# Kernel optimization log

Hardware: AMD Instinct MI355X
Metric: run time of the kernel (lower is better)

Reference implementation:

```python
import jax, jax.numpy as jnp
import numpy as np

VOCAB = 1_000_000   # vocabulary_size (num_classes)
EMB = 128           # embedding_size
NEG = 512           # number_of_negative_samples (num_sampled)
NTRUE = 1           # positive_samples (num_true)
BATCH = 16384


def _log_uniform_prob(ids, vocab):
    # TF LogUniformCandidateSampler: P(c) = (log(c+2) - log(c+1)) / log(vocab+1)
    c = ids.astype(jnp.float32)
    return (jnp.log(c + 2.0) - jnp.log(c + 1.0)) / jnp.log(float(vocab) + 1.0)


def _expected_count(ids, vocab, num_sampled):
    # unique sampling with num_sampled tries: E[count] = 1 - (1-p)^num_sampled
    p = _log_uniform_prob(ids, vocab)
    return -jnp.expm1(num_sampled * jnp.log1p(-p))


def _sigmoid_ce(logits, z):
    # stable sigmoid cross-entropy with label value z
    return jnp.maximum(logits, 0.0) - logits * z + jnp.log1p(jnp.exp(-jnp.abs(logits)))


def setup_inputs() -> dict:
    key = jax.random.key(0)
    k1, k2, k3, k4 = jax.random.split(key, 4)
    return {
        "predictions": jax.random.normal(k1, (BATCH, EMB), jnp.float32),
        "weights": jax.random.normal(k2, (VOCAB, EMB), jnp.float32) * 0.02,
        "biases": jnp.zeros((VOCAB,), jnp.float32),
        "labels": jax.random.randint(k3, (BATCH, NTRUE), 0, VOCAB, dtype=jnp.int64),
        "sampled": jax.random.randint(k4, (NEG,), 0, VOCAB, dtype=jnp.int64),
    }


def reference(predictions, weights, biases, labels, sampled):
    # --- true class logits: gather rows then batched dot ---
    true_w = weights[labels]                         # [B, T, E]
    true_b = biases[labels]                          # [B, T]
    true_logits = jnp.einsum('be,bte->bt', predictions, true_w) + true_b
    true_logits = true_logits - jnp.log(_expected_count(labels, VOCAB, NEG))

    # --- sampled (negative) class logits: shared across batch ---
    samp_logits = predictions @ weights[sampled].T + biases[sampled]  # [B, S]
    samp_logits = samp_logits - jnp.log(_expected_count(sampled, VOCAB, NEG))

    # --- sigmoid cross-entropy; true label value is 1/num_true ---
    loss_true = _sigmoid_ce(true_logits, jnp.float32(1.0 / NTRUE)).sum(axis=-1)
    loss_samp = _sigmoid_ce(samp_logits, jnp.float32(0.0)).sum(axis=-1)
    return jnp.mean(loss_true + loss_samp)
```

## Files before the change

kernel.cpp:

```cpp
#include <hip/hip_runtime.h>
#include <hip/hip_bf16.h>

#define VOCAB 1000000
#define EMB 128
#define NEG 512
#define BATCH 16384

#define BM 64
#define BN 64
#define KE 160
#define LDSTR 168

#define NMAIN ((BATCH / BM) * (NEG / BN))
#define NTRUE_BLK (BATCH / 4)
#define NPART (NMAIN + NTRUE_BLK)

typedef __attribute__((ext_vector_type(8))) short bf16x8;
typedef __attribute__((ext_vector_type(4))) float f32x4;

static __device__ __forceinline__ unsigned short f2bf(float f) {
    union { __hip_bfloat16 b; unsigned short u; } cv;
    cv.b = __float2bfloat16(f);
    return cv.u;
}
static __device__ __forceinline__ float bf2f(unsigned short u) {
    union { unsigned short u; __hip_bfloat16 b; } cv;
    cv.u = u;
    return __bfloat162float(cv.b);
}

static __device__ __forceinline__ float neg_log_expected(int c) {
    float cf = (float)c;
    float p = log1pf(1.0f / (cf + 1.0f)) / logf((float)VOCAB + 1.0f);
    float E = -expm1f((float)NEG * log1pf(-p));
    return -logf(E);
}

__global__ __launch_bounds__(64) void prep_k(const float* __restrict__ weights,
                                             const float* __restrict__ biases,
                                             const int* __restrict__ sampled,
                                             unsigned short* __restrict__ swe) {
    int s = blockIdx.x;
    int t = threadIdx.x;
    int sid = sampled[s];
    unsigned short* row = swe + (size_t)s * KE;
    if (t < 32) {
        const float4* src = (const float4*)(weights + (size_t)sid * EMB);
        float4 v = src[t];
        uint2 p;
        p.x = (unsigned)f2bf(v.x) | ((unsigned)f2bf(v.y) << 16);
        p.y = (unsigned)f2bf(v.z) | ((unsigned)f2bf(v.w) << 16);
        *(uint2*)(row + t * 4) = p;
    } else {
        int slot = 128 + (t - 32);
        unsigned short v = 0;
        if (slot <= 129) {
            float c = biases[sid] + neg_log_expected(sid);
            unsigned short hi = f2bf(c);
            v = (slot == 128) ? hi : f2bf(c - bf2f(hi));
        }
        row[slot] = v;
    }
}

__global__ __launch_bounds__(256) void main_k(const float* __restrict__ pred,
                                              const float* __restrict__ weights,
                                              const float* __restrict__ biases,
                                              const int* __restrict__ labels,
                                              const unsigned short* __restrict__ swe,
                                              float* __restrict__ partials) {
    __shared__ unsigned short As[BM * LDSTR];
    __shared__ unsigned short Bs[BN * LDSTR];
    __shared__ float red[4];
    int bid = blockIdx.x;
    int tid = threadIdx.x;
    int lane = tid & 63;
    int wv = tid >> 6;

    if (bid < NMAIN) {
        int m0 = (bid >> 3) * BM;
        int s0 = (bid & 7) * BN;

        const float4* pred4 = (const float4*)pred;
#pragma unroll
        for (int i = 0; i < 8; ++i) {
            int l = tid + i * 256;
            int row = l >> 5, k4 = l & 31;
            float4 v = pred4[(size_t)(m0 + row) * 32 + k4];
            uint2 p;
            p.x = (unsigned)f2bf(v.x) | ((unsigned)f2bf(v.y) << 16);
            p.y = (unsigned)f2bf(v.z) | ((unsigned)f2bf(v.w) << 16);
            *(uint2*)&As[row * LDSTR + k4 * 4] = p;
        }
#pragma unroll
        for (int i = 0; i < 8; ++i) {
            int l = tid + i * 256;
            int row = l >> 5, sl = l & 31;
            As[row * LDSTR + 128 + sl] = (sl < 2) ? (unsigned short)0x3F80 : (unsigned short)0;
        }
#pragma unroll
        for (int i = 0; i < 10; ++i) {
            int l = tid + i * 256;
            int row = l / 40, j = l % 40;
            uint2 p = ((const uint2*)(swe + (size_t)(s0 + row) * KE))[j];
            *(uint2*)&Bs[row * LDSTR + j * 4] = p;
        }
        __syncthreads();

        int wm = (wv & 1) * 32;
        int wn = (wv >> 1) * 32;
        int fr = lane & 15;
        int kq = (lane >> 4) * 8;

        f32x4 zero = {0.0f, 0.0f, 0.0f, 0.0f};
        f32x4 acc00 = zero, acc01 = zero, acc10 = zero, acc11 = zero;
#pragma unroll
        for (int kc = 0; kc < KE; kc += 32) {
            int kk = kc + kq;
            bf16x8 a0 = *(const bf16x8*)&As[(wm + fr) * LDSTR + kk];
            bf16x8 a1 = *(const bf16x8*)&As[(wm + 16 + fr) * LDSTR + kk];
            bf16x8 b0 = *(const bf16x8*)&Bs[(wn + fr) * LDSTR + kk];
            bf16x8 b1 = *(const bf16x8*)&Bs[(wn + 16 + fr) * LDSTR + kk];
            acc00 = __builtin_amdgcn_mfma_f32_16x16x32_bf16(a0, b0, acc00, 0, 0, 0);
            acc01 = __builtin_amdgcn_mfma_f32_16x16x32_bf16(a0, b1, acc01, 0, 0, 0);
            acc10 = __builtin_amdgcn_mfma_f32_16x16x32_bf16(a1, b0, acc10, 0, 0, 0);
            acc11 = __builtin_amdgcn_mfma_f32_16x16x32_bf16(a1, b1, acc11, 0, 0, 0);
        }
        float loss = 0.0f;
#pragma unroll
        for (int r = 0; r < 4; ++r) {
            float x;
            x = acc00[r]; loss += fmaxf(x, 0.0f) + log1pf(expf(-fabsf(x)));
            x = acc01[r]; loss += fmaxf(x, 0.0f) + log1pf(expf(-fabsf(x)));
            x = acc10[r]; loss += fmaxf(x, 0.0f) + log1pf(expf(-fabsf(x)));
            x = acc11[r]; loss += fmaxf(x, 0.0f) + log1pf(expf(-fabsf(x)));
        }
#pragma unroll
        for (int off = 32; off > 0; off >>= 1) loss += __shfl_xor(loss, off);
        if (lane == 0) red[wv] = loss;
        __syncthreads();
        if (tid == 0) partials[bid] = red[0] + red[1] + red[2] + red[3];
    } else {
        int b = (bid - NMAIN) * 4 + wv;
        int lbl = labels[b];
        float2 a = ((const float2*)pred)[(size_t)b * 64 + lane];
        float2 w = ((const float2*)weights)[(size_t)lbl * 64 + lane];
        float dot = a.x * w.x + a.y * w.y;
#pragma unroll
        for (int off = 32; off > 0; off >>= 1) dot += __shfl_xor(dot, off);
        if (lane == 0) {
            float x = dot + biases[lbl] + neg_log_expected(lbl);
            red[wv] = fmaxf(x, 0.0f) - x + log1pf(expf(-fabsf(x)));
        }
        __syncthreads();
        if (tid == 0) partials[bid] = red[0] + red[1] + red[2] + red[3];
    }
}

__global__ __launch_bounds__(256) void reduce_k(const float* __restrict__ partials,
                                                float* __restrict__ out) {
    int tid = threadIdx.x;
    float s = 0.0f;
    for (int i = tid; i < NPART; i += 256) s += partials[i];
#pragma unroll
    for (int off = 32; off > 0; off >>= 1) s += __shfl_xor(s, off);
    __shared__ float r[4];
    if ((tid & 63) == 0) r[tid >> 6] = s;
    __syncthreads();
    if (tid == 0) out[0] = (r[0] + r[1] + r[2] + r[3]) * (1.0f / (float)BATCH);
}

extern "C" void kernel_launch(void* const* d_in, const int* in_sizes, int n_in,
                              void* d_out, int out_size, void* d_ws, size_t ws_size,
                              hipStream_t stream) {
    const float* pred    = (const float*)d_in[0];
    const float* weights = (const float*)d_in[1];
    const float* biases  = (const float*)d_in[2];
    const int*   labels  = (const int*)d_in[3];
    const int*   sampled = (const int*)d_in[4];

    unsigned short* swe = (unsigned short*)d_ws;
    float* partials = (float*)((char*)d_ws + (size_t)NEG * KE * sizeof(unsigned short));
    float* out = (float*)d_out;

    prep_k<<<dim3(NEG), dim3(64), 0, stream>>>(weights, biases, sampled, swe);
    main_k<<<dim3(NPART), dim3(256), 0, stream>>>(pred, weights, biases, labels, swe, partials);
    reduce_k<<<dim3(1), dim3(256), 0, stream>>>(partials, out);
}
```

Before: 607.3 us.

## Fuse sampled-weight prep into main kernel and replace final reduction with atomics

Removes the separate prep kernel that gathered and converted the sampled weight rows to bf16. Each GEMM block now gathers its 64 sampled rows straight from the weight table and computes the bias and expected-count term itself. The partials buffer and final reduce kernel are replaced by a tiny zeroing kernel plus per-block float atomicAdd into the output. This cuts launches and a workspace round trip, but adds redundant gather and conversion work across the 256 M-tiles, 6144 contended atomics on one address, and a summation order that is no longer deterministic.

```diff
diff --git a/kernel.cpp b/kernel.cpp
--- a/kernel.cpp
+++ b/kernel.cpp
@@ -13,7 +13,7 @@
 
 #define NMAIN ((BATCH / BM) * (NEG / BN))
 #define NTRUE_BLK (BATCH / 4)
-#define NPART (NMAIN + NTRUE_BLK)
+#define NBLK (NMAIN + NTRUE_BLK)
 
 typedef __attribute__((ext_vector_type(8))) short bf16x8;
 typedef __attribute__((ext_vector_type(4))) float f32x4;
@@ -36,39 +36,16 @@
     return -logf(E);
 }
 
-__global__ __launch_bounds__(64) void prep_k(const float* __restrict__ weights,
-                                             const float* __restrict__ biases,
-                                             const int* __restrict__ sampled,
-                                             unsigned short* __restrict__ swe) {
-    int s = blockIdx.x;
-    int t = threadIdx.x;
-    int sid = sampled[s];
-    unsigned short* row = swe + (size_t)s * KE;
-    if (t < 32) {
-        const float4* src = (const float4*)(weights + (size_t)sid * EMB);
-        float4 v = src[t];
-        uint2 p;
-        p.x = (unsigned)f2bf(v.x) | ((unsigned)f2bf(v.y) << 16);
-        p.y = (unsigned)f2bf(v.z) | ((unsigned)f2bf(v.w) << 16);
-        *(uint2*)(row + t * 4) = p;
-    } else {
-        int slot = 128 + (t - 32);
-        unsigned short v = 0;
-        if (slot <= 129) {
-            float c = biases[sid] + neg_log_expected(sid);
-            unsigned short hi = f2bf(c);
-            v = (slot == 128) ? hi : f2bf(c - bf2f(hi));
-        }
-        row[slot] = v;
-    }
+__global__ __launch_bounds__(64) void zero_k(float* __restrict__ out) {
+    if (threadIdx.x == 0) out[0] = 0.0f;
 }
 
 __global__ __launch_bounds__(256) void main_k(const float* __restrict__ pred,
                                               const float* __restrict__ weights,
                                               const float* __restrict__ biases,
                                               const int* __restrict__ labels,
-                                              const unsigned short* __restrict__ swe,
-                                              float* __restrict__ partials) {
+                                              const int* __restrict__ sampled,
+                                              float* __restrict__ out) {
     __shared__ unsigned short As[BM * LDSTR];
     __shared__ unsigned short Bs[BN * LDSTR];
     __shared__ float red[4];
@@ -76,6 +53,8 @@
     int tid = threadIdx.x;
     int lane = tid & 63;
     int wv = tid >> 6;
+
+    const float inv_batch = 1.0f / (float)BATCH;
 
     if (bid < NMAIN) {
         int m0 = (bid >> 3) * BM;
@@ -98,12 +77,30 @@
             int row = l >> 5, sl = l & 31;
             As[row * LDSTR + 128 + sl] = (sl < 2) ? (unsigned short)0x3F80 : (unsigned short)0;
         }
+        const float4* w4 = (const float4*)weights;
 #pragma unroll
-        for (int i = 0; i < 10; ++i) {
+        for (int i = 0; i < 8; ++i) {
             int l = tid + i * 256;
-            int row = l / 40, j = l % 40;
-            uint2 p = ((const uint2*)(swe + (size_t)(s0 + row) * KE))[j];
-            *(uint2*)&Bs[row * LDSTR + j * 4] = p;
+            int row = l >> 5, k4 = l & 31;
+            int sid = sampled[s0 + row];
+            float4 v = w4[(size_t)sid * 32 + k4];
+            uint2 p;
+            p.x = (unsigned)f2bf(v.x) | ((unsigned)f2bf(v.y) << 16);
+            p.y = (unsigned)f2bf(v.z) | ((unsigned)f2bf(v.w) << 16);
+            *(uint2*)&Bs[row * LDSTR + k4 * 4] = p;
+        }
+#pragma unroll
+        for (int i = 0; i < 8; ++i) {
+            int l = tid + i * 256;
+            int row = l >> 5, sl = l & 31;
+            unsigned short v = 0;
+            if (sl < 2) {
+                int sid = sampled[s0 + row];
+                float c = biases[sid] + neg_log_expected(sid);
+                unsigned short hi = f2bf(c);
+                v = (sl == 0) ? hi : f2bf(c - bf2f(hi));
+            }
+            Bs[row * LDSTR + 128 + sl] = v;
         }
         __syncthreads();
 
@@ -139,7 +136,8 @@
         for (int off = 32; off > 0; off >>= 1) loss += __shfl_xor(loss, off);
         if (lane == 0) red[wv] = loss;
         __syncthreads();
-        if (tid == 0) partials[bid] = red[0] + red[1] + red[2] + red[3];
+        if (tid == 0)
+            atomicAdd(out, (red[0] + red[1] + red[2] + red[3]) * inv_batch);
     } else {
         int b = (bid - NMAIN) * 4 + wv;
         int lbl = labels[b];
@@ -153,21 +151,9 @@
             red[wv] = fmaxf(x, 0.0f) - x + log1pf(expf(-fabsf(x)));
         }
         __syncthreads();
-        if (tid == 0) partials[bid] = red[0] + red[1] + red[2] + red[3];
+        if (tid == 0)
+            atomicAdd(out, (red[0] + red[1] + red[2] + red[3]) * inv_batch);
     }
-}
-
-__global__ __launch_bounds__(256) void reduce_k(const float* __restrict__ partials,
-                                                float* __restrict__ out) {
-    int tid = threadIdx.x;
-    float s = 0.0f;
-    for (int i = tid; i < NPART; i += 256) s += partials[i];
-#pragma unroll
-    for (int off = 32; off > 0; off >>= 1) s += __shfl_xor(s, off);
-    __shared__ float r[4];
-    if ((tid & 63) == 0) r[tid >> 6] = s;
-    __syncthreads();
-    if (tid == 0) out[0] = (r[0] + r[1] + r[2] + r[3]) * (1.0f / (float)BATCH);
 }
 
 extern "C" void kernel_launch(void* const* d_in, const int* in_sizes, int n_in,
@@ -178,12 +164,10 @@
     const float* biases  = (const float*)d_in[2];
     const int*   labels  = (const int*)d_in[3];
     const int*   sampled = (const int*)d_in[4];
-
-    unsigned short* swe = (unsigned short*)d_ws;
-    float* partials = (float*)((char*)d_ws + (size_t)NEG * KE * sizeof(unsigned short));
     float* out = (float*)d_out;
 
-    prep_k<<<dim3(NEG), dim3(64), 0, stream>>>(weights, biases, sampled, swe);
-    main_k<<<dim3(NPART), dim3(256), 0, stream>>>(pred, weights, biases, labels, swe, partials);
-    reduce_k<<<dim3(1), dim3(256), 0, stream>>>(partials, out);
+    (void)d_ws; (void)ws_size;
+
+    zero_k<<<dim3(1), dim3(64), 0, stream>>>(out);
+    main_k<<<dim3(NBLK), dim3(256), 0, stream>>>(pred, weights, biases, labels, sampled, out);
 }
```

After: 666.3 us. 9.7% more time.
